# Kernel optimization log

Measured on AMD Instinct MI355X. Metric: run time of the kernel, lower is better.

Reference implementation:

```python
import math
import jax, jax.numpy as jnp
import numpy as np

B, C, H, W = 2, 256, 256, 256
TH, TW = 256, 256
U = V = 2            # window_size
PE_DIM = 256
DIM = 256
HEADS = 8
TEMP = 10000.0


def sine_pe(y, x, num_pos_feats, temp, card):
    """Faithful port of get_sine_position_encoding (use_norm=True)."""
    eps = 1e-6
    scale = 2.0 * math.pi
    y = y / (card[0] + eps) * scale
    x = x / (card[1] + eps) * scale
    dt = jnp.arange(num_pos_feats, dtype=jnp.float32)
    dim_t = temp ** (2.0 * jnp.floor(dt / 2.0) / num_pos_feats)
    px = x[..., None] / dim_t
    py = y[..., None] / dim_t

    def interleave(p):
        s = jnp.stack((jnp.sin(p[..., 0::2]), jnp.cos(p[..., 1::2])), axis=-1)
        return s.reshape(s.shape[:-2] + (-1,))

    return jnp.concatenate((interleave(py), interleave(px)), axis=-1)


def setup_inputs() -> dict:
    key = jax.random.key(0)
    ks = jax.random.split(key, 8)
    return {
        "feat_supp": jax.random.normal(ks[0], (B, C, H, W), jnp.float32),
        "offset": jax.random.normal(ks[1], (B, TH, TW, 2), jnp.float32) * 2.0,
        "Wq": jax.random.normal(ks[2], (DIM, PE_DIM), jnp.float32) * 0.02,
        "bq": jax.random.normal(ks[3], (DIM,), jnp.float32) * 0.02,
        "Wk": jax.random.normal(ks[4], (DIM, PE_DIM), jnp.float32) * 0.02,
        "bk": jax.random.normal(ks[5], (DIM,), jnp.float32) * 0.02,
        "Wv": jax.random.normal(ks[6], (DIM, PE_DIM), jnp.float32) * 0.02,
        "bv": jax.random.normal(ks[7], (DIM,), jnp.float32) * 0.02,
    }


def reference(feat_supp, offset, Wq, bq, Wk, bk, Wv, bv):
    UV = U * V
    THW = TH * TW
    Dh = DIM // HEADS
    attn_scale = Dh ** (-0.5)
    d = PE_DIM // C  # = 1 here

    # --- warp grid: integer window corners + fractional residual ---
    tgt = jnp.stack(jnp.meshgrid(jnp.arange(TH), jnp.arange(TW), indexing='ij'), axis=-1)  # [TH,TW,2]
    win = jnp.stack(jnp.meshgrid(jnp.arange(U), jnp.arange(V), indexing='ij'), axis=-1)    # [U,V,2]
    full = tgt[None].astype(jnp.float32) + offset[..., ::-1]            # [B,TH,TW,2]
    intg = jnp.floor(full).astype(jnp.int32)
    deci = (full - intg.astype(full.dtype)).reshape(B, THW, 2)          # fractional part
    idx = (intg[:, :, :, None, None, :] + win[None, None, None]).reshape(B, THW * UV, 2)

    # --- duplicate-padding gather (gather_hw) ---
    h_idx = jnp.clip(idx[..., 0], 0, H - 1)
    w_idx = jnp.clip(idx[..., 1], 0, W - 1)
    feat = feat_supp.transpose(0, 2, 3, 1).reshape(B, H * W, C)
    lin = h_idx * W + w_idx                                             # [B, THW*UV]
    feat_warp = jnp.take_along_axis(feat, lin[:, :, None], axis=1)      # [B, THW*UV, C]
    feat_warp_ori = feat_warp.reshape(B, THW, UV, C, 1)

    # --- sine PE on window coords (card = window_size - 1) ---
    ye, xe = jnp.meshgrid(jnp.arange(U, dtype=jnp.float32), jnp.arange(V, dtype=jnp.float32), indexing='ij')
    pos_bias = sine_pe(ye.reshape(1, -1), xe.reshape(1, -1), PE_DIM // 2, TEMP, (U - 1, V - 1))  # [1,UV,PE_DIM]
    pe_warp = pos_bias.reshape(1, 1, UV, C, d)
    fw = (feat_warp_ori + pe_warp).reshape(B, THW, UV, PE_DIM)

    # --- query features: window mean + sine PE of fractional offset (card = window_size) ---
    feat_base = feat_warp_ori[..., 0].mean(axis=2)                      # [B,THW,C]
    pe_curr = sine_pe(deci[..., 0], deci[..., 1], PE_DIM // 2, TEMP, (U, V)).reshape(B, THW, C, d)
    fb = (feat_base[..., None] + pe_curr).reshape(B, THW, PE_DIM)

    # --- cross attention: 1 query vs UV keys per target pixel ---
    q = (fb @ Wq.T + bq).reshape(B, THW, HEADS, Dh)
    k = (fw @ Wk.T + bk).reshape(B, THW, UV, HEADS, Dh)
    v = (fw @ Wv.T + bv).reshape(B, THW, UV, HEADS, Dh)
    attn = jnp.einsum('bthd,btuhd->bthu', q * attn_scale, k)
    attn = jax.nn.softmax(attn, axis=-1)
    out = jnp.einsum('bthu,btuhd->bthd', attn, v).reshape(B, TH, TW, DIM)
    return out.transpose(0, 3, 1, 2)                                    # [B, DIM, TH, TW]
```

## Files before the change

kernel.cpp:

```cpp
#include <hip/hip_runtime.h>


using short8 = __attribute__((ext_vector_type(8))) short;
using f32x4  = __attribute__((ext_vector_type(4))) float;
typedef unsigned short u16;

#define LOG2_1E4 13.287712379549449f
#define TWO_PI   6.283185307179586f

__device__ __forceinline__ float bs2f(u16 s) {
    unsigned u = ((unsigned)s) << 16;
    float f; __builtin_memcpy(&f, &u, 4); return f;
}
__device__ __forceinline__ u16 f2bs(float f) {
    unsigned u; __builtin_memcpy(&u, &f, 4);
    u += 0x7fffu + ((u >> 16) & 1u);
    return (u16)(u >> 16);
}

__device__ __forceinline__ int probe_is_f32(const u16* offs_raw) {
    const int lane = threadIdx.x & 63;
    const float v = bs2f(offs_raw[lane * 2]);
    const float av = fabsf(v);
    const bool insane = !(av >= 1e-3f && av <= 1000.0f);
    return __popcll(__ballot(insane)) >= 16 ? 1 : 0;
}

__global__ __launch_bounds__(256) void irm_canon(
    const void* offs_raw, const void* Wq_r, const void* bq_r,
    const void* Wk_r, const void* bk_r, const void* Wv_r, const void* bv_r,
    unsigned char* canon)
{
    const int is_f32 = probe_is_f32((const u16*)offs_raw);
    float* offsC = (float*)canon;
    u16* WqC = (u16*)(canon + (1u << 20));
    u16* WkC = (u16*)(canon + (1u << 20) + (1u << 17));
    u16* WvC = (u16*)(canon + (1u << 20) + (2u << 17));
    u16* bqC = (u16*)(canon + (1u << 20) + (3u << 17));
    u16* bkC = bqC + 256;
    u16* bvC = bkC + 256;

    const int gid = blockIdx.x * 256 + threadIdx.x;
    if (gid < 262144) {
        offsC[gid] = is_f32 ? ((const float*)offs_raw)[gid]
                            : bs2f(((const u16*)offs_raw)[gid]);
    } else if (gid < 262144 + 3 * 65536) {
        const int r = gid - 262144, w = r >> 16, i = r & 65535;
        const void* src = (w == 0) ? Wq_r : (w == 1) ? Wk_r : Wv_r;
        u16*       dst  = (w == 0) ? WqC  : (w == 1) ? WkC  : WvC;
        dst[i] = is_f32 ? f2bs(((const float*)src)[i]) : ((const u16*)src)[i];
    } else if (gid < 262144 + 3 * 65536 + 3 * 256) {
        const int r = gid - 262144 - 3 * 65536, w = r >> 8, i = r & 255;
        const void* src = (w == 0) ? bq_r : (w == 1) ? bk_r : bv_r;
        u16*       dst  = (w == 0) ? bqC  : (w == 1) ? bkC  : bvC;
        dst[i] = is_f32 ? f2bs(((const float*)src)[i]) : ((const u16*)src)[i];
    }
}

__global__ __launch_bounds__(256) void irm_transpose(const void* __restrict__ feat_raw,
                                                     const u16* __restrict__ offs_raw,
                                                     u16* __restrict__ featT) {
    const int is_f32 = probe_is_f32(offs_raw);
    __shared__ u16 tile[64][65];
    const int b   = blockIdx.z;
    const int c0  = blockIdx.y << 6;
    const int hw0 = blockIdx.x << 6;
    const int tid = threadIdx.x;
    const int r    = tid >> 4;
    const int col4 = (tid & 15) << 2;
    #pragma unroll
    for (int it = 0; it < 4; ++it) {
        const int c = (it << 4) + r;
        const size_t idx = ((size_t)((b << 8) + c0 + c) << 16) + hw0 + col4;
        if (is_f32) {
            float4 v = *(const float4*)((const float*)feat_raw + idx);
            tile[c][col4 + 0] = f2bs(v.x); tile[c][col4 + 1] = f2bs(v.y);
            tile[c][col4 + 2] = f2bs(v.z); tile[c][col4 + 3] = f2bs(v.w);
        } else {
            ushort4 v = *(const ushort4*)((const u16*)feat_raw + idx);
            tile[c][col4 + 0] = v.x; tile[c][col4 + 1] = v.y;
            tile[c][col4 + 2] = v.z; tile[c][col4 + 3] = v.w;
        }
    }
    __syncthreads();
    #pragma unroll
    for (int it = 0; it < 4; ++it) {
        const int hw = (it << 4) + r;
        ushort4 v;
        v.x = tile[col4 + 0][hw]; v.y = tile[col4 + 1][hw];
        v.z = tile[col4 + 2][hw]; v.w = tile[col4 + 3][hw];
        u16* dst = featT + ((size_t)((b << 16) + hw0 + hw) << 8) + c0 + col4;
        *(ushort4*)dst = v;
    }
}

__global__ __launch_bounds__(256, 2) void irm_main(
    const void* __restrict__ fsrc,
    const int transposed,
    const u16* __restrict__ offs_raw,
    const float* __restrict__ offsC,
    const u16* __restrict__ Wq, const u16* __restrict__ bq,
    const u16* __restrict__ Wk, const u16* __restrict__ bk,
    const u16* __restrict__ Wv, const u16* __restrict__ bv,
    void* __restrict__ out_raw)
{
    const int is_f32 = probe_is_f32(offs_raw);

    __shared__ __align__(16) unsigned char smem[56832];
    float* posb = (float*)(smem);
    u16*   sFw  = (u16*)(smem + 4096);
    u16*   sFb  = (u16*)(smem + 37888);
    u16*   sQ   = (u16*)(smem + 46336);
    float* sA   = (float*)(smem + 54784);
    u16*   sK   = (u16*)(smem);
    u16*   sV   = (u16*)(smem);

    const int tid = threadIdx.x;
    const int raw = blockIdx.x;
    const int wq_ = ((raw & 7) << 10) | (raw >> 3);
    const int b   = wq_ >> 12;
    const int t0  = (wq_ & 4095) << 4;

    {
        const int c = tid;
        const int j = (c & 127) >> 1;
        const float invt = exp2f(-(float)j * (LOG2_1E4 / 64.0f));
        const float sc = TWO_PI / (1.0f + 1e-6f);
        #pragma unroll
        for (int u = 0; u < 4; ++u) {
            const float base = (c < 128) ? (float)(u >> 1) : (float)(u & 1);
            const float arg = base * sc * invt;
            posb[u * 256 + c] = (c & 1) ? __cosf(arg) : __sinf(arg);
        }
    }
    __syncthreads();

    {
        const int p  = tid >> 4;
        const int cx = tid & 15;
        const int t  = t0 + p;
        const int ty = t >> 8, tx = t & 255;
        const float* op = offsC + (((size_t)b << 16) + (size_t)t) * 2;
        const float offx = op[0];
        const float offy = op[1];
        const float fy = (float)ty + offy;
        const float fx = (float)tx + offx;
        const float fiy = floorf(fy), fix = floorf(fx);
        const int iy = (int)fiy, ix = (int)fix;
        const float dy = fy - fiy, dx = fx - fix;

        float gsum[16];
        #pragma unroll
        for (int i = 0; i < 16; ++i) gsum[i] = 0.0f;

        #pragma unroll
        for (int u = 0; u < 4; ++u) {
            int hy = iy + (u >> 1); hy = hy < 0 ? 0 : (hy > 255 ? 255 : hy);
            int wx = ix + (u & 1);  wx = wx < 0 ? 0 : (wx > 255 ? 255 : wx);
            const int lin = (hy << 8) | wx;
            short8 g0, g1;
            if (transposed) {
                const u16* src = (const u16*)fsrc + (((size_t)(b << 16) + (size_t)lin) << 8) + (cx << 4);
                g0 = *(const short8*)(src);
                g1 = *(const short8*)(src + 8);
            } else {
                #pragma unroll
                for (int i = 0; i < 8; ++i) {
                    const size_t i0 = (((size_t)((b << 8) + (cx << 4) + i)) << 16) + lin;
                    const size_t i1 = (((size_t)((b << 8) + (cx << 4) + 8 + i)) << 16) + lin;
                    g0[i] = is_f32 ? (short)f2bs(((const float*)fsrc)[i0]) : (short)((const u16*)fsrc)[i0];
                    g1[i] = is_f32 ? (short)f2bs(((const float*)fsrc)[i1]) : (short)((const u16*)fsrc)[i1];
                }
            }
            short8 w0, w1;
            #pragma unroll
            for (int i = 0; i < 8; ++i) {
                const float f0 = bs2f((u16)g0[i]);
                const float f1 = bs2f((u16)g1[i]);
                gsum[i] += f0; gsum[i + 8] += f1;
                w0[i] = (short)f2bs(f0 + posb[u * 256 + (cx << 4) + i]);
                w1[i] = (short)f2bs(f1 + posb[u * 256 + (cx << 4) + 8 + i]);
            }
            *(short8*)&sFw[(p * 4 + u) * 264 + (cx << 4)]     = w0;
            *(short8*)&sFw[(p * 4 + u) * 264 + (cx << 4) + 8] = w1;
        }
        const float ys = dy * (TWO_PI / (2.0f + 1e-6f));
        const float xs = dx * (TWO_PI / (2.0f + 1e-6f));
        short8 q0, q1;
        #pragma unroll
        for (int i = 0; i < 16; ++i) {
            const int c = (cx << 4) + i;
            const int j = (c & 127) >> 1;
            const float invt = exp2f(-(float)j * (LOG2_1E4 / 64.0f));
            const float arg = ((c < 128) ? ys : xs) * invt;
            const float pe = (c & 1) ? __cosf(arg) : __sinf(arg);
            const float v = gsum[i] * 0.25f + pe;
            if (i < 8) q0[i] = (short)f2bs(v); else q1[i - 8] = (short)f2bs(v);
        }
        *(short8*)&sFb[p * 264 + (cx << 4)]     = q0;
        *(short8*)&sFb[p * 264 + (cx << 4) + 8] = q1;
    }
    __syncthreads();

    const int lane = tid & 63;
    const int wv   = tid >> 6;
    const int c15  = lane & 15;
    const int qd   = lane >> 4;
    const int colbase = wv << 6;
    const f32x4 zero4 = {0.f, 0.f, 0.f, 0.f};

    f32x4 accK[4][4], accV[4][4];
    #pragma unroll
    for (int m = 0; m < 4; ++m)
        #pragma unroll
        for (int nt = 0; nt < 4; ++nt) { accK[m][nt] = zero4; accV[m][nt] = zero4; }

    #pragma unroll
    for (int ks = 0; ks < 8; ++ks) {
        short8 af[4], bfr[4];
        #pragma unroll
        for (int m = 0; m < 4; ++m)
            af[m] = *(const short8*)&sFw[(m * 16 + c15) * 264 + ks * 32 + qd * 8];
        #pragma unroll
        for (int nt = 0; nt < 4; ++nt)
            bfr[nt] = *(const short8*)&Wk[(colbase + nt * 16 + c15) * 256 + ks * 32 + qd * 8];
        #pragma unroll
        for (int m = 0; m < 4; ++m)
            #pragma unroll
            for (int nt = 0; nt < 4; ++nt)
                accK[m][nt] = __builtin_amdgcn_mfma_f32_16x16x32_bf16(af[m], bfr[nt], accK[m][nt], 0, 0, 0);
    }

    {
        f32x4 accQ[4];
        #pragma unroll
        for (int nt = 0; nt < 4; ++nt) accQ[nt] = zero4;
        #pragma unroll
        for (int ks = 0; ks < 8; ++ks) {
            short8 aq = *(const short8*)&sFb[c15 * 264 + ks * 32 + qd * 8];
            #pragma unroll
            for (int nt = 0; nt < 4; ++nt) {
                short8 bw = *(const short8*)&Wq[(colbase + nt * 16 + c15) * 256 + ks * 32 + qd * 8];
                accQ[nt] = __builtin_amdgcn_mfma_f32_16x16x32_bf16(aq, bw, accQ[nt], 0, 0, 0);
            }
        }
        #pragma unroll
        for (int nt = 0; nt < 4; ++nt) {
            const int n = colbase + nt * 16 + c15;
            const float bias = bs2f(bq[n]);
            #pragma unroll
            for (int r = 0; r < 4; ++r)
                sQ[(qd * 4 + r) * 264 + n] = f2bs(accQ[nt][r] + bias);
        }
    }

    #pragma unroll
    for (int ks = 0; ks < 8; ++ks) {
        short8 af[4], bfr[4];
        #pragma unroll
        for (int m = 0; m < 4; ++m)
            af[m] = *(const short8*)&sFw[(m * 16 + c15) * 264 + ks * 32 + qd * 8];
        #pragma unroll
        for (int nt = 0; nt < 4; ++nt)
            bfr[nt] = *(const short8*)&Wv[(colbase + nt * 16 + c15) * 256 + ks * 32 + qd * 8];
        #pragma unroll
        for (int m = 0; m < 4; ++m)
            #pragma unroll
            for (int nt = 0; nt < 4; ++nt)
                accV[m][nt] = __builtin_amdgcn_mfma_f32_16x16x32_bf16(af[m], bfr[nt], accV[m][nt], 0, 0, 0);
    }

    __syncthreads();

    #pragma unroll
    for (int nt = 0; nt < 4; ++nt) {
        const int n = colbase + nt * 16 + c15;
        const float bias = bs2f(bk[n]);
        #pragma unroll
        for (int m = 0; m < 4; ++m)
            #pragma unroll
            for (int r = 0; r < 4; ++r)
                sK[(m * 16 + qd * 4 + r) * 264 + n] = f2bs(accK[m][nt][r] + bias);
    }
    __syncthreads();

    if (tid < 128) {
        const int p = tid & 15;
        const int h = tid >> 4;
        short8 q8[4];
        #pragma unroll
        for (int j = 0; j < 4; ++j)
            q8[j] = *(const short8*)&sQ[p * 264 + h * 32 + j * 8];
        float lg[4];
        #pragma unroll
        for (int u = 0; u < 4; ++u) {
            float acc = 0.0f;
            #pragma unroll
            for (int j = 0; j < 4; ++j) {
                short8 k8 = *(const short8*)&sK[(p * 4 + u) * 264 + h * 32 + j * 8];
                #pragma unroll
                for (int i = 0; i < 8; ++i)
                    acc += bs2f((u16)q8[j][i]) * bs2f((u16)k8[i]);
            }
            lg[u] = acc * 0.17677669529663687f;
        }
        const float mx = fmaxf(fmaxf(lg[0], lg[1]), fmaxf(lg[2], lg[3]));
        float e[4], es = 0.0f;
        #pragma unroll
        for (int u = 0; u < 4; ++u) { e[u] = __expf(lg[u] - mx); es += e[u]; }
        const float inv = __fdividef(1.0f, es);
        #pragma unroll
        for (int u = 0; u < 4; ++u)
            sA[((p << 3) + h) * 4 + u] = e[u] * inv;
    }
    __syncthreads();

    #pragma unroll
    for (int nt = 0; nt < 4; ++nt) {
        const int n = colbase + nt * 16 + c15;
        const float bias = bs2f(bv[n]);
        #pragma unroll
        for (int m = 0; m < 4; ++m)
            #pragma unroll
            for (int r = 0; r < 4; ++r)
                sV[(m * 16 + qd * 4 + r) * 264 + n] = f2bs(accV[m][nt][r] + bias);
    }
    __syncthreads();

    {
        const int p  = tid & 15;
        const int h  = (tid >> 4) & 7;
        const int dh = tid >> 7;
        float a4[4];
        #pragma unroll
        for (int u = 0; u < 4; ++u) a4[u] = sA[((p << 3) + h) * 4 + u];
        float acc[16];
        #pragma unroll
        for (int i = 0; i < 16; ++i) acc[i] = 0.0f;
        #pragma unroll
        for (int u = 0; u < 4; ++u) {
            const u16* vp = &sV[(p * 4 + u) * 264 + h * 32 + dh * 16];
            short8 v0 = *(const short8*)(vp);
            short8 v1 = *(const short8*)(vp + 8);
            #pragma unroll
            for (int i = 0; i < 8; ++i) {
                acc[i]     += a4[u] * bs2f((u16)v0[i]);
                acc[i + 8] += a4[u] * bs2f((u16)v1[i]);
            }
        }
        const size_t base = (((size_t)((b << 8) + h * 32 + dh * 16)) << 16) + t0 + p;
        if (is_f32) {
            float* dst = (float*)out_raw + base;
            #pragma unroll
            for (int i = 0; i < 16; ++i)
                dst[(size_t)i << 16] = acc[i];
        } else {
            u16* dst = (u16*)out_raw + base;
            #pragma unroll
            for (int i = 0; i < 16; ++i)
                dst[(size_t)i << 16] = f2bs(acc[i]);
        }
    }
}

extern "C" void kernel_launch(void* const* d_in, const int* in_sizes, int n_in,
                              void* d_out, int out_size, void* d_ws, size_t ws_size,
                              hipStream_t stream) {
    const size_t FEATT_BYTES = (size_t)1 << 26;
    const size_t CANON_BYTES = (1u << 20) + (3u << 17) + 3 * 512;
    const int use_t = (ws_size >= FEATT_BYTES + CANON_BYTES) ? 1 : 0;

    unsigned char* ws    = (unsigned char*)d_ws;
    unsigned char* canon = ws + (use_t ? FEATT_BYTES : 0);
    float* offsC = (float*)canon;
    u16* WqC = (u16*)(canon + (1u << 20));
    u16* WkC = (u16*)(canon + (1u << 20) + (1u << 17));
    u16* WvC = (u16*)(canon + (1u << 20) + (2u << 17));
    u16* bqC = (u16*)(canon + (1u << 20) + (3u << 17));
    u16* bkC = bqC + 256;
    u16* bvC = bkC + 256;

    irm_canon<<<1795, 256, 0, stream>>>(d_in[1], d_in[2], d_in[3], d_in[4],
                                        d_in[5], d_in[6], d_in[7], canon);
    if (use_t)
        irm_transpose<<<dim3(1024, 4, 2), 256, 0, stream>>>(d_in[0], (const u16*)d_in[1], (u16*)ws);
    irm_main<<<dim3(8192), 256, 0, stream>>>(use_t ? (const void*)ws : d_in[0], use_t,
                                             (const u16*)d_in[1], offsC,
                                             WqC, bqC, WkC, bkC, WvC, bvC, d_out);
}
```

Baseline: 692.6 us.

## Restructure attention kernel: fuse QK logits from MFMA accumulators, swizzle LDS, pack bf16

The main kernel now computes attention logits directly from the K MFMA accumulators dotted with Q via wave shuffles. This skips writing K to shared memory, dropping a sync phase and the K bias, which cancels in the softmax. Positional encoding is computed from one sin/cos table plus a per-channel inverse-frequency table instead of per-element exp2. Conversions use the hardware packed bf16 instruction, and LDS layouts for the transpose and V are XOR-swizzled. Launch bounds rise to 3 blocks with smaller shared memory, and outputs use nontemporal stores. The main risks are register pressure at higher occupancy and rounding differences from the packed bf16 conversion.

```diff
diff --git a/kernel.cpp b/kernel.cpp
--- a/kernel.cpp
+++ b/kernel.cpp
@@ -2,11 +2,13 @@
 
 
 using short8 = __attribute__((ext_vector_type(8))) short;
+using uint4v = __attribute__((ext_vector_type(4))) unsigned;
 using f32x4  = __attribute__((ext_vector_type(4))) float;
 typedef unsigned short u16;
 
 #define LOG2_1E4 13.287712379549449f
 #define TWO_PI   6.283185307179586f
+#define ATT_SCL  0.17677669529663687f
 
 __device__ __forceinline__ float bs2f(u16 s) {
     unsigned u = ((unsigned)s) << 16;
@@ -16,6 +18,11 @@
     unsigned u; __builtin_memcpy(&u, &f, 4);
     u += 0x7fffu + ((u >> 16) & 1u);
     return (u16)(u >> 16);
+}
+__device__ __forceinline__ unsigned cvt_pk_bf16(float lo, float hi) {
+    unsigned r;
+    asm("v_cvt_pk_bf16_f32 %0, %1, %2" : "=v"(r) : "v"(lo), "v"(hi));
+    return r;
 }
 
 __device__ __forceinline__ int probe_is_f32(const u16* offs_raw) {
@@ -61,7 +68,7 @@
                                                      const u16* __restrict__ offs_raw,
                                                      u16* __restrict__ featT) {
     const int is_f32 = probe_is_f32(offs_raw);
-    __shared__ u16 tile[64][65];
+    __shared__ u16 tile[64][72];
     const int b   = blockIdx.z;
     const int c0  = blockIdx.y << 6;
     const int hw0 = blockIdx.x << 6;
@@ -72,48 +79,55 @@
     for (int it = 0; it < 4; ++it) {
         const int c = (it << 4) + r;
         const size_t idx = ((size_t)((b << 8) + c0 + c) << 16) + hw0 + col4;
+        ushort4 o;
         if (is_f32) {
-            float4 v = *(const float4*)((const float*)feat_raw + idx);
-            tile[c][col4 + 0] = f2bs(v.x); tile[c][col4 + 1] = f2bs(v.y);
-            tile[c][col4 + 2] = f2bs(v.z); tile[c][col4 + 3] = f2bs(v.w);
+            const float4 v = *(const float4*)((const float*)feat_raw + idx);
+            const unsigned lo = cvt_pk_bf16(v.x, v.y);
+            const unsigned hi = cvt_pk_bf16(v.z, v.w);
+            o.x = (u16)(lo & 0xffffu); o.y = (u16)(lo >> 16);
+            o.z = (u16)(hi & 0xffffu); o.w = (u16)(hi >> 16);
         } else {
-            ushort4 v = *(const ushort4*)((const u16*)feat_raw + idx);
-            tile[c][col4 + 0] = v.x; tile[c][col4 + 1] = v.y;
-            tile[c][col4 + 2] = v.z; tile[c][col4 + 3] = v.w;
-        }
+            o = *(const ushort4*)((const u16*)feat_raw + idx);
+        }
+        *(ushort4*)&tile[c][col4 ^ (((c >> 3) & 7) << 3)] = o;
     }
     __syncthreads();
-    #pragma unroll
-    for (int it = 0; it < 4; ++it) {
-        const int hw = (it << 4) + r;
-        ushort4 v;
-        v.x = tile[col4 + 0][hw]; v.y = tile[col4 + 1][hw];
-        v.z = tile[col4 + 2][hw]; v.w = tile[col4 + 3][hw];
-        u16* dst = featT + ((size_t)((b << 16) + hw0 + hw) << 8) + c0 + col4;
-        *(ushort4*)dst = v;
-    }
-}
-
-__global__ __launch_bounds__(256, 2) void irm_main(
+    const int s = tid & 7;
+    const int m = tid >> 3;
+    #pragma unroll
+    for (int it2 = 0; it2 < 2; ++it2) {
+        const int hw = (it2 << 5) + m;
+        short8 o;
+        #pragma unroll
+        for (int k = 0; k < 8; ++k) {
+            const int c = (s << 3) + k;
+            o[k] = (short)tile[c][hw ^ (((c >> 3) & 7) << 3)];
+        }
+        u16* dst = featT + (((size_t)((b << 16) + hw0 + hw)) << 8) + c0 + (s << 3);
+        *(short8*)dst = o;
+    }
+}
+
+__global__ __launch_bounds__(256, 3) void irm_main(
     const void* __restrict__ fsrc,
     const int transposed,
     const u16* __restrict__ offs_raw,
     const float* __restrict__ offsC,
     const u16* __restrict__ Wq, const u16* __restrict__ bq,
-    const u16* __restrict__ Wk, const u16* __restrict__ bk,
+    const u16* __restrict__ Wk, const u16* __restrict__ bk_unused,
     const u16* __restrict__ Wv, const u16* __restrict__ bv,
     void* __restrict__ out_raw)
 {
     const int is_f32 = probe_is_f32(offs_raw);
 
-    __shared__ __align__(16) unsigned char smem[56832];
-    float* posb = (float*)(smem);
-    u16*   sFw  = (u16*)(smem + 4096);
-    u16*   sFb  = (u16*)(smem + 37888);
-    u16*   sQ   = (u16*)(smem + 46336);
-    float* sA   = (float*)(smem + 54784);
-    u16*   sK   = (u16*)(smem);
-    u16*   sV   = (u16*)(smem);
+    __shared__ __align__(16) unsigned char smem[52992];
+    float* pe1    = (float*)smem;
+    float* invtab = (float*)(smem + 1024);
+    float* sA     = (float*)smem;
+    u16*   sFw    = (u16*)(smem + 2304);
+    u16*   sV     = (u16*)(smem + 2304);
+    u16*   sFb    = (u16*)(smem + 36096);
+    u16*   sQ     = (u16*)(smem + 44544);
 
     const int tid = threadIdx.x;
     const int raw = blockIdx.x;
@@ -121,84 +135,115 @@
     const int b   = wq_ >> 12;
     const int t0  = (wq_ & 4095) << 4;
 
+    const int p0 = tid >> 4;
+    const int cx = tid & 15;
+    const int t  = t0 + p0;
+    const float offx = offsC[((((size_t)b << 16) + (size_t)t) << 1) + 0];
+    const float offy = offsC[((((size_t)b << 16) + (size_t)t) << 1) + 1];
+
     {
         const int c = tid;
         const int j = (c & 127) >> 1;
         const float invt = exp2f(-(float)j * (LOG2_1E4 / 64.0f));
-        const float sc = TWO_PI / (1.0f + 1e-6f);
-        #pragma unroll
-        for (int u = 0; u < 4; ++u) {
-            const float base = (c < 128) ? (float)(u >> 1) : (float)(u & 1);
-            const float arg = base * sc * invt;
-            posb[u * 256 + c] = (c & 1) ? __cosf(arg) : __sinf(arg);
-        }
+        const float arg = (TWO_PI / (1.0f + 1e-6f)) * invt;
+        pe1[c]    = (c & 1) ? __cosf(arg) : __sinf(arg);
+        invtab[c] = invt;
     }
     __syncthreads();
 
     {
-        const int p  = tid >> 4;
-        const int cx = tid & 15;
-        const int t  = t0 + p;
         const int ty = t >> 8, tx = t & 255;
-        const float* op = offsC + (((size_t)b << 16) + (size_t)t) * 2;
-        const float offx = op[0];
-        const float offy = op[1];
         const float fy = (float)ty + offy;
         const float fx = (float)tx + offx;
         const float fiy = floorf(fy), fix = floorf(fx);
         const int iy = (int)fiy, ix = (int)fix;
         const float dy = fy - fiy, dx = fx - fix;
 
-        float gsum[16];
-        #pragma unroll
-        for (int i = 0; i < 16; ++i) gsum[i] = 0.0f;
-
+        int lin4[4];
         #pragma unroll
         for (int u = 0; u < 4; ++u) {
             int hy = iy + (u >> 1); hy = hy < 0 ? 0 : (hy > 255 ? 255 : hy);
             int wx = ix + (u & 1);  wx = wx < 0 ? 0 : (wx > 255 ? 255 : wx);
-            const int lin = (hy << 8) | wx;
-            short8 g0, g1;
-            if (transposed) {
-                const u16* src = (const u16*)fsrc + (((size_t)(b << 16) + (size_t)lin) << 8) + (cx << 4);
-                g0 = *(const short8*)(src);
-                g1 = *(const short8*)(src + 8);
-            } else {
+            lin4[u] = (hy << 8) | wx;
+        }
+
+        short8 g[4][2];
+        if (transposed) {
+            #pragma unroll
+            for (int u = 0; u < 4; ++u) {
+                const u16* src = (const u16*)fsrc +
+                    ((((size_t)(b << 16)) + (size_t)lin4[u]) << 8) + (cx << 4);
+                g[u][0] = *(const short8*)(src);
+                g[u][1] = *(const short8*)(src + 8);
+            }
+        } else {
+            #pragma unroll
+            for (int u = 0; u < 4; ++u) {
                 #pragma unroll
                 for (int i = 0; i < 8; ++i) {
-                    const size_t i0 = (((size_t)((b << 8) + (cx << 4) + i)) << 16) + lin;
-                    const size_t i1 = (((size_t)((b << 8) + (cx << 4) + 8 + i)) << 16) + lin;
-                    g0[i] = is_f32 ? (short)f2bs(((const float*)fsrc)[i0]) : (short)((const u16*)fsrc)[i0];
-                    g1[i] = is_f32 ? (short)f2bs(((const float*)fsrc)[i1]) : (short)((const u16*)fsrc)[i1];
+                    const size_t i0 = (((size_t)((b << 8) + (cx << 4) + i)) << 16) + lin4[u];
+                    const size_t i1 = (((size_t)((b << 8) + (cx << 4) + 8 + i)) << 16) + lin4[u];
+                    g[u][0][i] = is_f32 ? (short)f2bs(((const float*)fsrc)[i0]) : (short)((const u16*)fsrc)[i0];
+                    g[u][1][i] = is_f32 ? (short)f2bs(((const float*)fsrc)[i1]) : (short)((const u16*)fsrc)[i1];
                 }
             }
-            short8 w0, w1;
-            #pragma unroll
-            for (int i = 0; i < 8; ++i) {
-                const float f0 = bs2f((u16)g0[i]);
-                const float f1 = bs2f((u16)g1[i]);
-                gsum[i] += f0; gsum[i + 8] += f1;
-                w0[i] = (short)f2bs(f0 + posb[u * 256 + (cx << 4) + i]);
-                w1[i] = (short)f2bs(f1 + posb[u * 256 + (cx << 4) + 8 + i]);
-            }
-            *(short8*)&sFw[(p * 4 + u) * 264 + (cx << 4)]     = w0;
-            *(short8*)&sFw[(p * 4 + u) * 264 + (cx << 4) + 8] = w1;
-        }
+        }
+
+        float pe1v[16], invtv[16];
+        #pragma unroll
+        for (int i = 0; i < 16; ++i) {
+            pe1v[i]  = pe1[(cx << 4) + i];
+            invtv[i] = invtab[(cx << 4) + i];
+        }
+
+        const bool hi_half = (cx >= 8);
+        float gsum[16];
+        #pragma unroll
+        for (int i = 0; i < 16; ++i) gsum[i] = 0.0f;
+
+        #pragma unroll
+        for (int u = 0; u < 4; ++u) {
+            const bool sel = hi_half ? (bool)(u & 1) : (bool)(u >> 1);
+            unsigned pk[8];
+            #pragma unroll
+            for (int i2 = 0; i2 < 8; ++i2) {
+                float w2[2];
+                #pragma unroll
+                for (int k = 0; k < 2; ++k) {
+                    const int i = i2 * 2 + k;
+                    const float f = bs2f((u16)g[u][i >> 3][i & 7]);
+                    gsum[i] += f;
+                    const float pz = (i & 1) ? 1.0f : 0.0f;
+                    w2[k] = f + (sel ? pe1v[i] : pz);
+                }
+                pk[i2] = cvt_pk_bf16(w2[0], w2[1]);
+            }
+            const uint4v lo = {pk[0], pk[1], pk[2], pk[3]};
+            const uint4v hi = {pk[4], pk[5], pk[6], pk[7]};
+            *(uint4v*)&sFw[((p0 << 2) + u) * 264 + (cx << 4)]     = lo;
+            *(uint4v*)&sFw[((p0 << 2) + u) * 264 + (cx << 4) + 8] = hi;
+        }
+
         const float ys = dy * (TWO_PI / (2.0f + 1e-6f));
         const float xs = dx * (TWO_PI / (2.0f + 1e-6f));
-        short8 q0, q1;
-        #pragma unroll
-        for (int i = 0; i < 16; ++i) {
-            const int c = (cx << 4) + i;
-            const int j = (c & 127) >> 1;
-            const float invt = exp2f(-(float)j * (LOG2_1E4 / 64.0f));
-            const float arg = ((c < 128) ? ys : xs) * invt;
-            const float pe = (c & 1) ? __cosf(arg) : __sinf(arg);
-            const float v = gsum[i] * 0.25f + pe;
-            if (i < 8) q0[i] = (short)f2bs(v); else q1[i - 8] = (short)f2bs(v);
-        }
-        *(short8*)&sFb[p * 264 + (cx << 4)]     = q0;
-        *(short8*)&sFb[p * 264 + (cx << 4) + 8] = q1;
+        const float sxy = hi_half ? xs : ys;
+        unsigned qk[8];
+        #pragma unroll
+        for (int i2 = 0; i2 < 8; ++i2) {
+            float v2[2];
+            #pragma unroll
+            for (int k = 0; k < 2; ++k) {
+                const int i = i2 * 2 + k;
+                const float arg = sxy * invtv[i];
+                const float pe = (i & 1) ? __cosf(arg) : __sinf(arg);
+                v2[k] = gsum[i] * 0.25f + pe;
+            }
+            qk[i2] = cvt_pk_bf16(v2[0], v2[1]);
+        }
+        const uint4v qlo = {qk[0], qk[1], qk[2], qk[3]};
+        const uint4v qhi = {qk[4], qk[5], qk[6], qk[7]};
+        *(uint4v*)&sFb[p0 * 264 + (cx << 4)]     = qlo;
+        *(uint4v*)&sFb[p0 * 264 + (cx << 4) + 8] = qhi;
     }
     __syncthreads();
 
@@ -209,28 +254,6 @@
     const int colbase = wv << 6;
     const f32x4 zero4 = {0.f, 0.f, 0.f, 0.f};
 
-    f32x4 accK[4][4], accV[4][4];
-    #pragma unroll
-    for (int m = 0; m < 4; ++m)
-        #pragma unroll
-        for (int nt = 0; nt < 4; ++nt) { accK[m][nt] = zero4; accV[m][nt] = zero4; }
-
-    #pragma unroll
-    for (int ks = 0; ks < 8; ++ks) {
-        short8 af[4], bfr[4];
-        #pragma unroll
-        for (int m = 0; m < 4; ++m)
-            af[m] = *(const short8*)&sFw[(m * 16 + c15) * 264 + ks * 32 + qd * 8];
-        #pragma unroll
-        for (int nt = 0; nt < 4; ++nt)
-            bfr[nt] = *(const short8*)&Wk[(colbase + nt * 16 + c15) * 256 + ks * 32 + qd * 8];
-        #pragma unroll
-        for (int m = 0; m < 4; ++m)
-            #pragma unroll
-            for (int nt = 0; nt < 4; ++nt)
-                accK[m][nt] = __builtin_amdgcn_mfma_f32_16x16x32_bf16(af[m], bfr[nt], accK[m][nt], 0, 0, 0);
-    }
-
     {
         f32x4 accQ[4];
         #pragma unroll
@@ -249,11 +272,20 @@
             const int n = colbase + nt * 16 + c15;
             const float bias = bs2f(bq[n]);
             #pragma unroll
-            for (int r = 0; r < 4; ++r)
-                sQ[(qd * 4 + r) * 264 + n] = f2bs(accQ[nt][r] + bias);
-        }
-    }
-
+            for (int rp = 0; rp < 2; ++rp) {
+                const unsigned pk = cvt_pk_bf16(accQ[nt][2 * rp] + bias, accQ[nt][2 * rp + 1] + bias);
+                sQ[(qd * 4 + 2 * rp)     * 264 + n] = (u16)(pk & 0xffffu);
+                sQ[(qd * 4 + 2 * rp + 1) * 264 + n] = (u16)(pk >> 16);
+            }
+        }
+    }
+    asm volatile("" ::: "memory");
+
+    f32x4 accK[4][4];
+    #pragma unroll
+    for (int m = 0; m < 4; ++m)
+        #pragma unroll
+        for (int nt = 0; nt < 4; ++nt) accK[m][nt] = zero4;
     #pragma unroll
     for (int ks = 0; ks < 8; ++ks) {
         short8 af[4], bfr[4];
@@ -262,56 +294,79 @@
             af[m] = *(const short8*)&sFw[(m * 16 + c15) * 264 + ks * 32 + qd * 8];
         #pragma unroll
         for (int nt = 0; nt < 4; ++nt)
+            bfr[nt] = *(const short8*)&Wk[(colbase + nt * 16 + c15) * 256 + ks * 32 + qd * 8];
+        #pragma unroll
+        for (int m = 0; m < 4; ++m)
+            #pragma unroll
+            for (int nt = 0; nt < 4; ++nt)
+                accK[m][nt] = __builtin_amdgcn_mfma_f32_16x16x32_bf16(af[m], bfr[nt], accK[m][nt], 0, 0, 0);
+    }
+
+    {
+        float part[4][4][2];
+        #pragma unroll
+        for (int m = 0; m < 4; ++m)
+            #pragma unroll
+            for (int r = 0; r < 4; ++r) { part[m][r][0] = 0.f; part[m][r][1] = 0.f; }
+        #pragma unroll
+        for (int m = 0; m < 4; ++m) {
+            #pragma unroll
+            for (int nt = 0; nt < 4; ++nt) {
+                const float qv = bs2f(sQ[(4 * m + qd) * 264 + colbase + nt * 16 + c15]);
+                #pragma unroll
+                for (int r = 0; r < 4; ++r)
+                    part[m][r][nt >> 1] += accK[m][nt][r] * qv;
+            }
+        }
+        #pragma unroll
+        for (int m = 0; m < 4; ++m)
+            #pragma unroll
+            for (int r = 0; r < 4; ++r)
+                #pragma unroll
+                for (int h2 = 0; h2 < 2; ++h2) {
+                    float v = part[m][r][h2];
+                    v += __shfl_xor(v, 1);
+                    v += __shfl_xor(v, 2);
+                    v += __shfl_xor(v, 4);
+                    v += __shfl_xor(v, 8);
+                    part[m][r][h2] = v;
+                }
+        auto smax_write = [&](const float (&pm)[4][2], const int p) {
+            #pragma unroll
+            for (int h2 = 0; h2 < 2; ++h2) {
+                const float l0 = pm[0][h2] * ATT_SCL, l1 = pm[1][h2] * ATT_SCL;
+                const float l2 = pm[2][h2] * ATT_SCL, l3 = pm[3][h2] * ATT_SCL;
+                const float mx = fmaxf(fmaxf(l0, l1), fmaxf(l2, l3));
+                const float e0 = __expf(l0 - mx), e1 = __expf(l1 - mx);
+                const float e2 = __expf(l2 - mx), e3 = __expf(l3 - mx);
+                const float inv = __fdividef(1.0f, e0 + e1 + e2 + e3);
+                float* ap = &sA[p * 36 + ((wv << 1) + h2) * 4];
+                ap[0] = e0 * inv; ap[1] = e1 * inv; ap[2] = e2 * inv; ap[3] = e3 * inv;
+            }
+        };
+        if      (c15 == 0) { smax_write(part[0], qd);     smax_write(part[1], 4 + qd);  }
+        else if (c15 == 8) { smax_write(part[2], 8 + qd); smax_write(part[3], 12 + qd); }
+    }
+
+    f32x4 accV[4][4];
+    #pragma unroll
+    for (int m = 0; m < 4; ++m)
+        #pragma unroll
+        for (int nt = 0; nt < 4; ++nt) accV[m][nt] = zero4;
+    #pragma unroll
+    for (int ks = 0; ks < 8; ++ks) {
+        short8 af[4], bfr[4];
+        #pragma unroll
+        for (int m = 0; m < 4; ++m)
+            af[m] = *(const short8*)&sFw[(m * 16 + c15) * 264 + ks * 32 + qd * 8];
+        #pragma unroll
+        for (int nt = 0; nt < 4; ++nt)
             bfr[nt] = *(const short8*)&Wv[(colbase + nt * 16 + c15) * 256 + ks * 32 + qd * 8];
         #pragma unroll
         for (int m = 0; m < 4; ++m)
             #pragma unroll
             for (int nt = 0; nt < 4; ++nt)
                 accV[m][nt] = __builtin_amdgcn_mfma_f32_16x16x32_bf16(af[m], bfr[nt], accV[m][nt], 0, 0, 0);
-    }
-
-    __syncthreads();
-
-    #pragma unroll
-    for (int nt = 0; nt < 4; ++nt) {
-        const int n = colbase + nt * 16 + c15;
-        const float bias = bs2f(bk[n]);
-        #pragma unroll
-        for (int m = 0; m < 4; ++m)
-            #pragma unroll
-            for (int r = 0; r < 4; ++r)
-                sK[(m * 16 + qd * 4 + r) * 264 + n] = f2bs(accK[m][nt][r] + bias);
-    }
-    __syncthreads();
-
-    if (tid < 128) {
-        const int p = tid & 15;
-        const int h = tid >> 4;
-        short8 q8[4];
-        #pragma unroll
-        for (int j = 0; j < 4; ++j)
-            q8[j] = *(const short8*)&sQ[p * 264 + h * 32 + j * 8];
-        float lg[4];
-        #pragma unroll
-        for (int u = 0; u < 4; ++u) {
-            float acc = 0.0f;
-            #pragma unroll
-            for (int j = 0; j < 4; ++j) {
-                short8 k8 = *(const short8*)&sK[(p * 4 + u) * 264 + h * 32 + j * 8];
-                #pragma unroll
-                for (int i = 0; i < 8; ++i)
-                    acc += bs2f((u16)q8[j][i]) * bs2f((u16)k8[i]);
-            }
-            lg[u] = acc * 0.17677669529663687f;
-        }
-        const float mx = fmaxf(fmaxf(lg[0], lg[1]), fmaxf(lg[2], lg[3]));
-        float e[4], es = 0.0f;
-        #pragma unroll
-        for (int u = 0; u < 4; ++u) { e[u] = __expf(lg[u] - mx); es += e[u]; }
-        const float inv = __fdividef(1.0f, es);
-        #pragma unroll
-        for (int u = 0; u < 4; ++u)
-            sA[((p << 3) + h) * 4 + u] = e[u] * inv;
     }
     __syncthreads();
 
@@ -320,10 +375,16 @@
         const int n = colbase + nt * 16 + c15;
         const float bias = bs2f(bv[n]);
         #pragma unroll
-        for (int m = 0; m < 4; ++m)
-            #pragma unroll
-            for (int r = 0; r < 4; ++r)
-                sV[(m * 16 + qd * 4 + r) * 264 + n] = f2bs(accV[m][nt][r] + bias);
+        for (int m = 0; m < 4; ++m) {
+            #pragma unroll
+            for (int rp = 0; rp < 2; ++rp) {
+                const int row = m * 16 + qd * 4 + 2 * rp;
+                const int ns = n ^ (((row >> 2) & 7) << 3);
+                const unsigned pk = cvt_pk_bf16(accV[m][nt][2 * rp] + bias, accV[m][nt][2 * rp + 1] + bias);
+                sV[row * 264 + ns]       = (u16)(pk & 0xffffu);
+                sV[(row + 1) * 264 + ns] = (u16)(pk >> 16);
+            }
+        }
     }
     __syncthreads();
 
@@ -331,21 +392,22 @@
         const int p  = tid & 15;
         const int h  = (tid >> 4) & 7;
         const int dh = tid >> 7;
-        float a4[4];
-        #pragma unroll
-        for (int u = 0; u < 4; ++u) a4[u] = sA[((p << 3) + h) * 4 + u];
+        const f32x4 a4 = *(const f32x4*)&sA[p * 36 + h * 4];
         float acc[16];
         #pragma unroll
         for (int i = 0; i < 16; ++i) acc[i] = 0.0f;
         #pragma unroll
         for (int u = 0; u < 4; ++u) {
-            const u16* vp = &sV[(p * 4 + u) * 264 + h * 32 + dh * 16];
-            short8 v0 = *(const short8*)(vp);
-            short8 v1 = *(const short8*)(vp + 8);
+            const int row = p * 4 + u;
+            const int f = ((row >> 2) & 7) << 3;
+            const int cb = h * 32 + dh * 16;
+            const short8 v0 = *(const short8*)&sV[row * 264 + (cb ^ f)];
+            const short8 v1 = *(const short8*)&sV[row * 264 + ((cb + 8) ^ f)];
+            const float a = a4[u];
             #pragma unroll
             for (int i = 0; i < 8; ++i) {
-                acc[i]     += a4[u] * bs2f((u16)v0[i]);
-                acc[i + 8] += a4[u] * bs2f((u16)v1[i]);
+                acc[i]     += a * bs2f((u16)v0[i]);
+                acc[i + 8] += a * bs2f((u16)v1[i]);
             }
         }
         const size_t base = (((size_t)((b << 8) + h * 32 + dh * 16)) << 16) + t0 + p;
@@ -353,12 +415,12 @@
             float* dst = (float*)out_raw + base;
             #pragma unroll
             for (int i = 0; i < 16; ++i)
-                dst[(size_t)i << 16] = acc[i];
+                __builtin_nontemporal_store(acc[i], dst + ((size_t)i << 16));
         } else {
             u16* dst = (u16*)out_raw + base;
             #pragma unroll
             for (int i = 0; i < 16; ++i)
-                dst[(size_t)i << 16] = f2bs(acc[i]);
+                __builtin_nontemporal_store(f2bs(acc[i]), dst + ((size_t)i << 16));
         }
     }
 }
```

Result: faster. 610.6 us (-11.8%).
